# Performance work log

Hardware: AMD Instinct MI355X
Metric: run time of the kernel (lower is better)

## Reference

```python
import jax, jax.numpy as jnp
import numpy as np

B, H, S, D = 8, 8, 2048, 64
NEG = -1e9


def setup_inputs() -> dict:
    key = jax.random.key(0)
    k1, k2, k3, k4 = jax.random.split(key, 4)
    query = jax.random.normal(k1, (B, H, S, D), dtype=jnp.float32)
    kk = jax.random.normal(k2, (B, H, S, D), dtype=jnp.float32)
    value = jax.random.normal(k3, (B, H, S, D), dtype=jnp.float32)
    mask = jax.random.randint(k4, (B, S, S), 0, 2, dtype=jnp.int32)
    return {"query": query, "key": kk, "value": value, "mask": mask}


def reference(query, key, value, mask):
    dk = key.shape[-1]
    # scores: [B,H,S,S] = (q/sqrt(dk)) @ k^T
    scores = jnp.einsum('bhqd,bhkd->bhqk', query / np.sqrt(dk), key)
    # mask broadcast over heads: [B,1,S,S]
    scores = jnp.where(mask[:, None, :, :] == 0, NEG, scores)
    attn = jax.nn.softmax(scores.astype(jnp.float32), axis=-1).astype(query.dtype)
    # dropout is identity in eval/deterministic reference
    return jnp.einsum('bhqk,bhkd->bhqd', attn, value)
```

## Files before the change

### kernel.cpp

```cpp
#include <hip/hip_runtime.h>
#include <hip/hip_bf16.h>
#include <stdint.h>


#define B_ 8
#define H_ 8
#define S_ 2048
#define D_ 64
#define QT 128
#define KT 64
#define NT (S_ / KT)
#define LOG2E 1.44269504088896340736f
#define QSCALE (0.125f * LOG2E)

typedef __bf16 bf16;
typedef bf16 bf16x8 __attribute__((ext_vector_type(8)));
typedef float f32x4 __attribute__((ext_vector_type(4)));
typedef unsigned short ushort8_t __attribute__((ext_vector_type(8)));
typedef unsigned long long u64;

#if __has_builtin(__builtin_amdgcn_exp2f)
#define EXP2(x) __builtin_amdgcn_exp2f(x)
#else
#define EXP2(x) exp2f(x)
#endif

static __device__ __forceinline__ unsigned short bfb(float f) {
    bf16 h = (bf16)f;
    return __builtin_bit_cast(unsigned short, h);
}
static __device__ __forceinline__ int phi_inv(int c) {
    return ((c >> 5) & 1) * 32 + ((c >> 2) & 1) * 16 + ((c >> 4) & 1) * 8 +
           ((c >> 3) & 1) * 4 + (c & 3);
}
static __device__ __forceinline__ void gload16(const unsigned short* g, unsigned short* l) {
    __builtin_amdgcn_global_load_lds(
        (const __attribute__((address_space(1))) unsigned int*)g,
        (__attribute__((address_space(3))) unsigned int*)l, 16, 0, 0);
}

#define KV_BLOCKS (B_ * H_ * NT)

__global__ __launch_bounds__(256) void prep_fused(
    const float* __restrict__ K, const float* __restrict__ V,
    unsigned short* __restrict__ Ko, unsigned short* __restrict__ Vo,
    const int* __restrict__ M, u64* __restrict__ W) {
    const int tid = threadIdx.x;
    if (blockIdx.x >= KV_BLOCKS) {
        const int ln = tid & 63;
        const int w0 = (blockIdx.x - KV_BLOCKS) * 32 + (tid >> 6) * 8;
#pragma unroll
        for (int j = 0; j < 8; ++j) {
            const int v = M[(long)(w0 + j) * 64 + ln];
            const u64 bal = __ballot(v != 0);
            if (ln == 0) W[w0 + j] = bal;
        }
        return;
    }
    if (Ko == nullptr) return;
    __shared__ float Vl[64][65];
    const int t = blockIdx.x & (NT - 1);
    const int bh = blockIdx.x >> 5;
    const float* Kg = K + ((long)bh * S_ + t * 64) * D_;
    const float* Vg = V + ((long)bh * S_ + t * 64) * D_;
    unsigned short* Kout = Ko + ((long)bh * S_ + t * 64) * D_;
    unsigned short* Vout = Vo + (long)bh * D_ * S_ + t * 64;
    {
        const int kv = tid >> 2, d0 = (tid & 3) * 16;
#pragma unroll
        for (int half = 0; half < 2; ++half) {
            const float4 f0 = *(const float4*)(Kg + kv * D_ + d0 + half * 8);
            const float4 f1 = *(const float4*)(Kg + kv * D_ + d0 + half * 8 + 4);
            ushort8_t u;
            u[0] = bfb(f0.x); u[1] = bfb(f0.y); u[2] = bfb(f0.z); u[3] = bfb(f0.w);
            u[4] = bfb(f1.x); u[5] = bfb(f1.y); u[6] = bfb(f1.z); u[7] = bfb(f1.w);
            *(ushort8_t*)(Kout + kv * D_ + d0 + half * 8) = u;
        }
    }
    {
#pragma unroll
        for (int i = 0; i < 4; ++i) {
            const int kv = i * 16 + (tid >> 4);
            const int d4 = (tid & 15) * 4;
            const float4 f = *(const float4*)(Vg + kv * D_ + d4);
            Vl[kv][d4 + 0] = f.x; Vl[kv][d4 + 1] = f.y;
            Vl[kv][d4 + 2] = f.z; Vl[kv][d4 + 3] = f.w;
        }
    }
    __syncthreads();
    {
#pragma unroll
        for (int j = 0; j < 4; ++j) {
            const int chunk = j * 256 + tid;
            const int d = chunk >> 4, q4 = chunk & 15;
            ushort4 w;
            w.x = bfb(Vl[phi_inv(q4 * 4 + 0)][d]);
            w.y = bfb(Vl[phi_inv(q4 * 4 + 1)][d]);
            w.z = bfb(Vl[phi_inv(q4 * 4 + 2)][d]);
            w.w = bfb(Vl[phi_inv(q4 * 4 + 3)][d]);
            *(ushort4*)(Vout + (long)d * S_ + q4 * 4) = w;
        }
    }
}

template <int MODE>
__global__ __launch_bounds__(512, 4) void attn_fwd(
    const float* __restrict__ Q, const float* __restrict__ K,
    const float* __restrict__ V, const int* __restrict__ M,
    const u64* __restrict__ W, const unsigned short* __restrict__ Kp,
    const unsigned short* __restrict__ Vp, float* __restrict__ O)
{
    __shared__ __attribute__((aligned(16))) unsigned short Ks[2][KT * D_];
    __shared__ __attribute__((aligned(16))) unsigned short Vt[2][D_ * KT];

    const int tid = threadIdx.x;
    const int wv = tid >> 6, ln = tid & 63;
    const int col = ln & 15, grp = ln >> 4;

    int bid = blockIdx.x;
    bid = (bid & 7) * 128 + (bid >> 3);
    const int qt = bid & 15;
    const int h = (bid >> 4) & 7;
    const int b = bid >> 7;
    const int qw = qt * QT + wv * 16;

    const float* Qg = Q + ((long)((b * H_ + h) * S_) + qw + col) * D_;
    bf16x8 qf[2];
#pragma unroll
    for (int c = 0; c < 2; ++c) {
        const float4 a0 = *(const float4*)(Qg + c * 32 + grp * 8);
        const float4 a1 = *(const float4*)(Qg + c * 32 + grp * 8 + 4);
        qf[c][0] = (bf16)(a0.x * QSCALE); qf[c][1] = (bf16)(a0.y * QSCALE);
        qf[c][2] = (bf16)(a0.z * QSCALE); qf[c][3] = (bf16)(a0.w * QSCALE);
        qf[c][4] = (bf16)(a1.x * QSCALE); qf[c][5] = (bf16)(a1.y * QSCALE);
        qf[c][6] = (bf16)(a1.z * QSCALE); qf[c][7] = (bf16)(a1.w * QSCALE);
    }
    bf16x8 onesf;
#pragma unroll
    for (int j = 0; j < 8; ++j) onesf[j] = (bf16)1.0f;

    f32x4 oacc[4];
#pragma unroll
    for (int i = 0; i < 4; ++i) oacc[i] = (f32x4){0.f, 0.f, 0.f, 0.f};
    f32x4 accs = (f32x4){0.f, 0.f, 0.f, 0.f};

    const u64* Wg = (MODE >= 1) ? (W + ((long)b * S_ + qw + col) * (S_ / 64)) : nullptr;
    const int* Mg = (MODE == 0) ? (M + ((long)b * S_ + qw + col) * S_) : nullptr;
    const unsigned short* Kbh = Kp + (long)(b * H_ + h) * S_ * D_;
    const unsigned short* Vbh = Vp + (long)(b * H_ + h) * D_ * S_;
    const float* Kf = K + (long)(b * H_ + h) * S_ * D_;
    const float* Vf = V + (long)(b * H_ + h) * S_ * D_;

    const int rl = ln >> 3;
    const int c8 = (ln & 7) ^ rl;
    const int krow = wv * 8 + rl;

    float4 ka[2];
    float va[8];
    const int vd = ln, kg0 = wv;

    auto STAGE_ISSUE = [&](int kv0, int buf) {
        gload16(Kbh + (long)(kv0 + krow) * D_ + c8 * 8, &Ks[buf][0] + wv * 512);
        gload16(Vbh + (long)krow * S_ + kv0 + c8 * 8, &Vt[buf][0] + wv * 512);
    };
    auto LOADT = [&](int kv0) {
#pragma unroll
        for (int i = 0; i < 2; ++i) {
            const int idx4 = i * 512 + tid;
            const int row = idx4 >> 4, c4 = idx4 & 15;
            ka[i] = *(const float4*)(Kf + (long)(kv0 + row) * D_ + c4 * 4);
        }
#pragma unroll
        for (int i = 0; i < 2; ++i) {
            const int kg = kg0 + i * 8;
            const int kvn = phi_inv(kg * 4);
#pragma unroll
            for (int j = 0; j < 4; ++j)
                va[i * 4 + j] = Vf[(long)(kv0 + kvn + j) * D_ + vd];
        }
    };
    auto WRITET = [&](int buf) {
#pragma unroll
        for (int i = 0; i < 2; ++i) {
            const int idx4 = i * 512 + tid;
            const int row = idx4 >> 4, c4 = idx4 & 15;
            const int byte = (row * 128 + c4 * 8) ^ ((row & 7) << 4);
            ushort4 w;
            w.x = bfb(ka[i].x); w.y = bfb(ka[i].y);
            w.z = bfb(ka[i].z); w.w = bfb(ka[i].w);
            *(ushort4*)((char*)Ks[buf] + byte) = w;
        }
#pragma unroll
        for (int i = 0; i < 2; ++i) {
            const int kg = kg0 + i * 8;
            const int byte = (vd * 128 + kg * 8) ^ ((vd & 7) << 4);
            ushort4 w;
            w.x = bfb(va[i * 4 + 0]); w.y = bfb(va[i * 4 + 1]);
            w.z = bfb(va[i * 4 + 2]); w.w = bfb(va[i * 4 + 3]);
            *(ushort4*)((char*)Vt[buf] + byte) = w;
        }
    };

    auto STEP = [&](int t, const unsigned short* Kc, const unsigned short* Vc) {
        u64 mws = 0;
        if (MODE >= 1) mws = Wg[t] >> (grp * 4);
        f32x4 sc[4];
        __builtin_amdgcn_s_setprio(1);
#pragma unroll
        for (int blk = 0; blk < 4; ++blk) {
            sc[blk] = (f32x4){0.f, 0.f, 0.f, 0.f};
#pragma unroll
            for (int c = 0; c < 2; ++c) {
                const int row = blk * 16 + col;
                const int byte = (row * 128 + c * 64 + grp * 16) ^ ((row & 7) << 4);
                const bf16x8 kf = *(const bf16x8*)((const char*)Kc + byte);
                sc[blk] = __builtin_amdgcn_mfma_f32_16x16x32_bf16(kf, qf[c], sc[blk], 0, 0, 0);
            }
        }
        __builtin_amdgcn_s_setprio(0);
        bf16x8 pf[2];
        if (MODE >= 1) {
            const unsigned mlo = (unsigned)mws, mhi = (unsigned)(mws >> 32);
#pragma unroll
            for (int c = 0; c < 2; ++c)
#pragma unroll
                for (int j = 0; j < 8; ++j) {
                    const int blk = 2 * c + (j >> 2), r = j & 3;
                    const unsigned w32 = (blk < 2) ? mlo : mhi;
                    const int bit = (blk & 1) * 16 + r;
                    const float s = ((w32 >> bit) & 1u) ? sc[blk][r] : -1e9f;
                    pf[c][j] = (bf16)EXP2(s);
                }
        } else {
#pragma unroll
            for (int c = 0; c < 2; ++c)
#pragma unroll
                for (int j = 0; j < 8; ++j) {
                    const int blk = 2 * c + (j >> 2), r = j & 3;
                    const int mv = Mg[t * KT + blk * 16 + grp * 4 + r];
                    const float s = mv ? sc[blk][r] : -1e9f;
                    pf[c][j] = (bf16)EXP2(s);
                }
        }
        __builtin_amdgcn_s_setprio(1);
        accs = __builtin_amdgcn_mfma_f32_16x16x32_bf16(pf[0], onesf, accs, 0, 0, 0);
        accs = __builtin_amdgcn_mfma_f32_16x16x32_bf16(pf[1], onesf, accs, 0, 0, 0);
#pragma unroll
        for (int c = 0; c < 2; ++c)
#pragma unroll
            for (int db = 0; db < 4; ++db) {
                const int vrow = db * 16 + col;
                const int byte = (vrow * 128 + c * 64 + grp * 16) ^ ((vrow & 7) << 4);
                const bf16x8 vf = *(const bf16x8*)((const char*)Vc + byte);
                oacc[db] = __builtin_amdgcn_mfma_f32_16x16x32_bf16(pf[c], vf, oacc[db], 0, 0, 0);
            }
        __builtin_amdgcn_s_setprio(0);
    };

    if (MODE == 2) {
        STAGE_ISSUE(0, 0);
    } else {
        LOADT(0);
        WRITET(0);
    }
    __syncthreads();

#pragma unroll 1
    for (int t = 0; t < NT; t += 2) {
        if (t + 1 < NT) {
            if (MODE == 2) STAGE_ISSUE((t + 1) * KT, 1);
            else LOADT((t + 1) * KT);
        }
        STEP(t, Ks[0], Vt[0]);
        if (MODE < 2 && t + 1 < NT) WRITET(1);
        __syncthreads();
        if (t + 2 < NT) {
            if (MODE == 2) STAGE_ISSUE((t + 2) * KT, 0);
            else LOADT((t + 2) * KT);
        }
        STEP(t + 1, Ks[1], Vt[1]);
        if (MODE < 2 && t + 2 < NT) WRITET(0);
        __syncthreads();
    }

    float* Og = O + ((long)((b * H_ + h) * S_) + qw) * D_;
#pragma unroll
    for (int r = 0; r < 4; ++r) {
        const float inv = 1.0f / accs[r];
#pragma unroll
        for (int db = 0; db < 4; ++db)
            Og[(grp * 4 + r) * D_ + db * 16 + col] = oacc[db][r] * inv;
    }
}

extern "C" void kernel_launch(void* const* d_in, const int* in_sizes, int n_in,
                              void* d_out, int out_size, void* d_ws, size_t ws_size,
                              hipStream_t stream) {
    (void)in_sizes; (void)n_in; (void)out_size;
    const float* Q = (const float*)d_in[0];
    const float* K = (const float*)d_in[1];
    const float* V = (const float*)d_in[2];
    const int*   M = (const int*)d_in[3];
    float* O = (float*)d_out;

    const size_t szW = (size_t)B_ * S_ * (S_ / 64) * sizeof(u64);
    const size_t szK = (size_t)B_ * H_ * S_ * D_ * 2;
    const int grid = B_ * H_ * (S_ / QT);
    const int nmaskblk = (B_ * S_ * (S_ / 64)) / 32;

    if (ws_size >= szW + 2 * szK) {
        u64* W = (u64*)d_ws;
        unsigned short* Kp = (unsigned short*)((char*)d_ws + szW);
        unsigned short* Vp = (unsigned short*)((char*)d_ws + szW + szK);
        prep_fused<<<KV_BLOCKS + nmaskblk, 256, 0, stream>>>(K, V, Kp, Vp, M, W);
        attn_fwd<2><<<grid, 512, 0, stream>>>(Q, K, V, M, W, Kp, Vp, O);
    } else if (ws_size >= szW) {
        u64* W = (u64*)d_ws;
        prep_fused<<<KV_BLOCKS + nmaskblk, 256, 0, stream>>>(K, V, nullptr, nullptr, M, W);
        attn_fwd<1><<<grid, 512, 0, stream>>>(Q, K, V, M, W, nullptr, nullptr, O);
    } else {
        attn_fwd<0><<<grid, 512, 0, stream>>>(Q, K, V, M, nullptr, nullptr, nullptr, O);
    }
}
```

Baseline: 160.6 us.

## Deepen K/V async staging to a 4-slot ring with prefetch distance two

For the direct-to-LDS load mode, K/V tiles now rotate through a 4-slot shared-memory ring, with loads issued two tiles ahead. Each step waits with a partial vmcnt(2) plus a raw barrier instead of a full __syncthreads, so global loads can overlap more compute. The mask word is loaded before the stage issue, and the first score MFMA starts from a zero constant. LDS use doubles (64 KB per block), which may lower occupancy below the launch-bounds target of 4 blocks.

```diff
diff --git a/kernel.cpp b/kernel.cpp
--- a/kernel.cpp
+++ b/kernel.cpp
@@ -10,6 +10,7 @@
 #define QT 128
 #define KT 64
 #define NT (S_ / KT)
+#define TILE_E (KT * D_)
 #define LOG2E 1.44269504088896340736f
 #define QSCALE (0.125f * LOG2E)
 
@@ -110,8 +111,8 @@
     const u64* __restrict__ W, const unsigned short* __restrict__ Kp,
     const unsigned short* __restrict__ Vp, float* __restrict__ O)
 {
-    __shared__ __attribute__((aligned(16))) unsigned short Ks[2][KT * D_];
-    __shared__ __attribute__((aligned(16))) unsigned short Vt[2][D_ * KT];
+    __shared__ __attribute__((aligned(16))) unsigned short Ks3[4 * TILE_E];
+    __shared__ __attribute__((aligned(16))) unsigned short Vt3[4 * TILE_E];
 
     const int tid = threadIdx.x;
     const int wv = tid >> 6, ln = tid & 63;
@@ -138,11 +139,12 @@
     bf16x8 onesf;
 #pragma unroll
     for (int j = 0; j < 8; ++j) onesf[j] = (bf16)1.0f;
+    const f32x4 zq = (f32x4){0.f, 0.f, 0.f, 0.f};
 
     f32x4 oacc[4];
 #pragma unroll
-    for (int i = 0; i < 4; ++i) oacc[i] = (f32x4){0.f, 0.f, 0.f, 0.f};
-    f32x4 accs = (f32x4){0.f, 0.f, 0.f, 0.f};
+    for (int i = 0; i < 4; ++i) oacc[i] = zq;
+    f32x4 accs = zq;
 
     const u64* Wg = (MODE >= 1) ? (W + ((long)b * S_ + qw + col) * (S_ / 64)) : nullptr;
     const int* Mg = (MODE == 0) ? (M + ((long)b * S_ + qw + col) * S_) : nullptr;
@@ -160,8 +162,8 @@
     const int vd = ln, kg0 = wv;
 
     auto STAGE_ISSUE = [&](int kv0, int buf) {
-        gload16(Kbh + (long)(kv0 + krow) * D_ + c8 * 8, &Ks[buf][0] + wv * 512);
-        gload16(Vbh + (long)krow * S_ + kv0 + c8 * 8, &Vt[buf][0] + wv * 512);
+        gload16(Kbh + (long)(kv0 + krow) * D_ + c8 * 8, Ks3 + buf * TILE_E + wv * 512);
+        gload16(Vbh + (long)krow * S_ + kv0 + c8 * 8, Vt3 + buf * TILE_E + wv * 512);
     };
     auto LOADT = [&](int kv0) {
 #pragma unroll
@@ -188,7 +190,7 @@
             ushort4 w;
             w.x = bfb(ka[i].x); w.y = bfb(ka[i].y);
             w.z = bfb(ka[i].z); w.w = bfb(ka[i].w);
-            *(ushort4*)((char*)Ks[buf] + byte) = w;
+            *(ushort4*)((char*)(Ks3 + buf * TILE_E) + byte) = w;
         }
 #pragma unroll
         for (int i = 0; i < 2; ++i) {
@@ -197,29 +199,27 @@
             ushort4 w;
             w.x = bfb(va[i * 4 + 0]); w.y = bfb(va[i * 4 + 1]);
             w.z = bfb(va[i * 4 + 2]); w.w = bfb(va[i * 4 + 3]);
-            *(ushort4*)((char*)Vt[buf] + byte) = w;
+            *(ushort4*)((char*)(Vt3 + buf * TILE_E) + byte) = w;
         }
     };
 
-    auto STEP = [&](int t, const unsigned short* Kc, const unsigned short* Vc) {
-        u64 mws = 0;
-        if (MODE >= 1) mws = Wg[t] >> (grp * 4);
+    auto STEP = [&](u64 mwfull, int t, const unsigned short* Kc, const unsigned short* Vc) {
         f32x4 sc[4];
         __builtin_amdgcn_s_setprio(1);
 #pragma unroll
         for (int blk = 0; blk < 4; ++blk) {
-            sc[blk] = (f32x4){0.f, 0.f, 0.f, 0.f};
-#pragma unroll
-            for (int c = 0; c < 2; ++c) {
-                const int row = blk * 16 + col;
-                const int byte = (row * 128 + c * 64 + grp * 16) ^ ((row & 7) << 4);
-                const bf16x8 kf = *(const bf16x8*)((const char*)Kc + byte);
-                sc[blk] = __builtin_amdgcn_mfma_f32_16x16x32_bf16(kf, qf[c], sc[blk], 0, 0, 0);
-            }
+            const int row = blk * 16 + col;
+            const int byte0 = (row * 128 + grp * 16) ^ ((row & 7) << 4);
+            const int byte1 = (row * 128 + 64 + grp * 16) ^ ((row & 7) << 4);
+            const bf16x8 kf0 = *(const bf16x8*)((const char*)Kc + byte0);
+            const bf16x8 kf1 = *(const bf16x8*)((const char*)Kc + byte1);
+            sc[blk] = __builtin_amdgcn_mfma_f32_16x16x32_bf16(kf0, qf[0], zq, 0, 0, 0);
+            sc[blk] = __builtin_amdgcn_mfma_f32_16x16x32_bf16(kf1, qf[1], sc[blk], 0, 0, 0);
         }
         __builtin_amdgcn_s_setprio(0);
         bf16x8 pf[2];
         if (MODE >= 1) {
+            const u64 mws = mwfull >> (grp * 4);
             const unsigned mlo = (unsigned)mws, mhi = (unsigned)(mws >> 32);
 #pragma unroll
             for (int c = 0; c < 2; ++c)
@@ -257,30 +257,56 @@
         __builtin_amdgcn_s_setprio(0);
     };
 
+#define WAIT2_BAR() do { asm volatile("s_waitcnt vmcnt(2)" ::: "memory"); \
+    __builtin_amdgcn_s_barrier(); __builtin_amdgcn_sched_barrier(0); } while (0)
+#define WAIT0_BAR() do { asm volatile("s_waitcnt vmcnt(0)" ::: "memory"); \
+    __builtin_amdgcn_s_barrier(); __builtin_amdgcn_sched_barrier(0); } while (0)
+
     if (MODE == 2) {
         STAGE_ISSUE(0, 0);
+        STAGE_ISSUE(KT, 1);
+        WAIT2_BAR();
+#pragma unroll 1
+        for (int tt = 0; tt + 4 < NT; tt += 4) {
+#pragma unroll
+            for (int j = 0; j < 4; ++j) {
+                const int t = tt + j;
+                const u64 mw = Wg[t];
+                STAGE_ISSUE((t + 2) * KT, (j + 2) & 3);
+                STEP(mw, t, Ks3 + j * TILE_E, Vt3 + j * TILE_E);
+                WAIT2_BAR();
+            }
+        }
+        {
+            const u64 mw0 = Wg[NT - 4];
+            STAGE_ISSUE((NT - 2) * KT, (NT - 2) & 3);
+            STEP(mw0, NT - 4, Ks3 + ((NT - 4) & 3) * TILE_E, Vt3 + ((NT - 4) & 3) * TILE_E);
+            WAIT2_BAR();
+            const u64 mw1 = Wg[NT - 3];
+            STAGE_ISSUE((NT - 1) * KT, (NT - 1) & 3);
+            STEP(mw1, NT - 3, Ks3 + ((NT - 3) & 3) * TILE_E, Vt3 + ((NT - 3) & 3) * TILE_E);
+            WAIT2_BAR();
+            const u64 mw2 = Wg[NT - 2];
+            STEP(mw2, NT - 2, Ks3 + ((NT - 2) & 3) * TILE_E, Vt3 + ((NT - 2) & 3) * TILE_E);
+            WAIT0_BAR();
+            const u64 mw3 = Wg[NT - 1];
+            STEP(mw3, NT - 1, Ks3 + ((NT - 1) & 3) * TILE_E, Vt3 + ((NT - 1) & 3) * TILE_E);
+        }
     } else {
         LOADT(0);
         WRITET(0);
-    }
-    __syncthreads();
-
+        __syncthreads();
 #pragma unroll 1
-    for (int t = 0; t < NT; t += 2) {
-        if (t + 1 < NT) {
-            if (MODE == 2) STAGE_ISSUE((t + 1) * KT, 1);
-            else LOADT((t + 1) * KT);
-        }
-        STEP(t, Ks[0], Vt[0]);
-        if (MODE < 2 && t + 1 < NT) WRITET(1);
-        __syncthreads();
-        if (t + 2 < NT) {
-            if (MODE == 2) STAGE_ISSUE((t + 2) * KT, 0);
-            else LOADT((t + 2) * KT);
-        }
-        STEP(t + 1, Ks[1], Vt[1]);
-        if (MODE < 2 && t + 2 < NT) WRITET(0);
-        __syncthreads();
+        for (int t = 0; t < NT; t += 2) {
+            if (t + 1 < NT) LOADT((t + 1) * KT);
+            STEP(MODE >= 1 ? Wg[t] : 0ull, t, Ks3, Vt3);
+            if (t + 1 < NT) WRITET(1);
+            __syncthreads();
+            if (t + 2 < NT) LOADT((t + 2) * KT);
+            STEP(MODE >= 1 ? Wg[t + 1] : 0ull, t + 1, Ks3 + TILE_E, Vt3 + TILE_E);
+            if (t + 2 < NT) WRITET(0);
+            __syncthreads();
+        }
     }
 
     float* Og = O + ((long)((b * H_ + h) * S_) + qw) * D_;
@@ -291,6 +317,8 @@
         for (int db = 0; db < 4; ++db)
             Og[(grp * 4 + r) * D_ + db * 16 + col] = oacc[db][r] * inv;
     }
+#undef WAIT2_BAR
+#undef WAIT0_BAR
 }
 
 extern "C" void kernel_launch(void* const* d_in, const int* in_sizes, int n_in,
```

New measurement: 155.6 us (median of 2 runs). -3.1%, faster.
